# Optimization experiments

Measured on AMD Instinct MI355X. Metric: run time of the kernel, lower is better.

## Reference

```python
import jax, jax.numpy as jnp
import numpy as np

B_, L_, DM, DI, N, R, K = 2, 1024, 1024, 2048, 16, 64, 4
EPS = 1e-5

def silu(x):
    return x * jax.nn.sigmoid(x)

def causal_conv1d(x, w, b):
    # x: (B,L,D); w: (D,K) depthwise. torch Conv1d(padding=K-1) then slice [:L] == left-pad causal conv.
    L = x.shape[1]
    xp = jnp.pad(x, ((0, 0), (K - 1, 0), (0, 0)))
    y = xp[:, 0:L, :] * w[:, 0]
    for k in range(1, K):
        y = y + xp[:, k:k + L, :] * w[:, k]
    return y + b

def selective_scan(u, delta, A, Bm, Cm, D):
    # u, delta: (B,L,D); A: (D,N); Bm, Cm: (B,L,N)
    dA = jnp.exp(jnp.einsum('bld,dn->bldn', delta, A))
    dBu = jnp.einsum('bld,bln,bld->bldn', delta, Bm, u)
    h0 = jnp.zeros((u.shape[0], u.shape[2], A.shape[1]), u.dtype)
    def step(h, xs):
        dA_t, dBu_t, C_t = xs
        h = dA_t * h + dBu_t
        return h, jnp.einsum('bdn,bn->bd', h, C_t)
    _, ys = jax.lax.scan(step, h0, (jnp.moveaxis(dA, 1, 0), jnp.moveaxis(dBu, 1, 0), jnp.moveaxis(Cm, 1, 0)))
    return jnp.moveaxis(ys, 0, 1) + u * D  # (B,L,D)

def branch(x, conv_w, conv_b, Wx, Wdt, bdt, A_log, D):
    x = silu(causal_conv1d(x, conv_w, conv_b))
    dbl = x @ Wx.T                               # (B,L,R+2N)
    dt, Bm, Cm = dbl[..., :R], dbl[..., R:R + N], dbl[..., R + N:]
    dt = dt @ Wdt.T + bdt                        # dt_proj is Linear WITH bias in source
    delta = jax.nn.softplus(dt + bdt)            # source also passes delta_bias to the scan (bias added twice; faithful)
    A = -jnp.exp(A_log)
    return selective_scan(x, delta, A, Bm, Cm, D)

def reference(a, b, Wi, conv_w, conv_b, Wx, Wdt, bdt, A_log, D,
              conv_w_b, conv_b_b, Wx_b, Wdt_b, bdt_b, A_log_b, D_b, Wo, norm_w):
    xz_a = a @ Wi.T
    x_f, z = xz_a[..., :DI], xz_a[..., DI:]
    y_f = branch(x_f, conv_w, conv_b, Wx, Wdt, bdt, A_log, D)
    xz_b = jnp.flip(b, 1) @ Wi.T
    x_bwd = xz_b[..., :DI]
    y_b = jnp.flip(branch(x_bwd, conv_w_b, conv_b_b, Wx_b, Wdt_b, bdt_b, A_log_b, D_b), 1)
    y = y_f + y_b
    # RMSNormGated, norm_before_gate=False: gate first, then RMSNorm
    g = y * silu(z)
    g = g * jax.lax.rsqrt(jnp.mean(g * g, axis=-1, keepdims=True) + EPS) * norm_w
    return g @ Wo.T

def setup_inputs() -> dict:
    key = jax.random.key(0)
    ks = jax.random.split(key, 16)
    s = 0.02
    def rn(k, shape):
        return jax.random.normal(k, shape, jnp.float32) * s
    def inv_dt(k):
        dt = jnp.exp(jax.random.uniform(k, (DI,)) * (np.log(0.1) - np.log(0.001)) + np.log(0.001))
        dt = jnp.clip(dt, 1e-4, None)
        return dt + jnp.log(-jnp.expm1(-dt))
    A_log = jnp.log(jnp.broadcast_to(jnp.arange(1, N + 1, dtype=jnp.float32), (DI, N)))
    return dict(
        a=jax.random.normal(ks[0], (B_, L_, DM), jnp.float32),
        b=jax.random.normal(ks[1], (B_, L_, DM), jnp.float32),
        Wi=rn(ks[2], (2 * DI, DM)),
        conv_w=rn(ks[3], (DI, K)), conv_b=rn(ks[4], (DI,)),
        Wx=rn(ks[5], (R + 2 * N, DI)), Wdt=rn(ks[6], (DI, R)), bdt=inv_dt(ks[7]),
        A_log=A_log, D=jnp.ones((DI,), jnp.float32),
        conv_w_b=rn(ks[8], (DI, K)), conv_b_b=rn(ks[9], (DI,)),
        Wx_b=rn(ks[10], (R + 2 * N, DI)), Wdt_b=rn(ks[11], (DI, R)), bdt_b=inv_dt(ks[12]),
        A_log_b=A_log, D_b=jnp.ones((DI,), jnp.float32),
        Wo=rn(ks[13], (DM, DI)), norm_w=jnp.ones((DI,), jnp.float32),
    )
```

## Files before the change

### kernel.cpp

```cpp
#include <hip/hip_runtime.h>
#include <hip/hip_bf16.h>
#include <cmath>

#define B_ 2
#define L_ 1024
#define DM 1024
#define DI 2048
#define NS 16
#define RR 64
#define KC 4
#define NCH 64
#define CL (L_ / NCH)
#define NSPLIT 16

using frag8 = __attribute__((ext_vector_type(8))) short;
using facc4 = __attribute__((ext_vector_type(4))) float;

struct alignas(8) S4 { short x, y, z, w; };

__device__ __forceinline__ short f2b(float v) {
    __hip_bfloat16 h = __float2bfloat16(v);
    return *(short*)&h;
}

__device__ __forceinline__ float silu1(float x) {
    return x / (1.f + __expf(-x));
}

__device__ __forceinline__ void pow_tree(float q, float* pw) {
    float q2 = q * q, q4 = q2 * q2, q8 = q4 * q4;
    pw[0] = q;        pw[1] = q2;       pw[2] = q2 * q;   pw[3] = q4;
    pw[4] = q4 * q;   pw[5] = q4 * q2;  pw[6] = q4 * pw[2]; pw[7] = q8;
    pw[8] = q8 * q;   pw[9] = q8 * q2;  pw[10] = q8 * pw[2]; pw[11] = q8 * q4;
    pw[12] = q8 * pw[4]; pw[13] = q8 * pw[5]; pw[14] = q8 * pw[6]; pw[15] = q8 * q8;
}

__device__ __forceinline__ void async_ld16(const void* g, void* l) {
    __builtin_amdgcn_global_load_lds(
        (const __attribute__((address_space(1))) unsigned int*)g,
        (__attribute__((address_space(3))) unsigned int*)l, 16, 0, 0);
}

__device__ __forceinline__ void cvt4(const float* __restrict__ src, size_t si,
                                     short* __restrict__ dst, size_t di2) {
    float4 v = *(const float4*)(src + si);
    S4 r = { f2b(v.x), f2b(v.y), f2b(v.z), f2b(v.w) };
    *(S4*)(dst + di2) = r;
}

__global__ void cvt_all(const float* __restrict__ a, const float* __restrict__ b,
                        const float* __restrict__ Wi,
                        const float* __restrict__ Wx, const float* __restrict__ Wxb2,
                        const float* __restrict__ Wdt, const float* __restrict__ Wdtb2,
                        const float* __restrict__ Wo,
                        short* __restrict__ abf, short* __restrict__ bbf,
                        short* __restrict__ Wibf,
                        short* __restrict__ Wxbf, short* __restrict__ Wxbbf,
                        short* __restrict__ Wdtbf, short* __restrict__ Wdtbbf,
                        short* __restrict__ Wobf) {
    size_t i = ((size_t)blockIdx.x * 256 + threadIdx.x) * 4;
    const size_t S_ab = (size_t)B_ * L_ * DM;
    if (i < S_ab) { cvt4(a, i, abf, i); return; } i -= S_ab;
    if (i < S_ab) {
        size_t r = i / DM, c = i % DM;
        size_t bb = r / L_, ll = r % L_;
        size_t sr = bb * L_ + (L_ - 1 - ll);
        cvt4(b, sr * DM + c, bbf, i); return;
    } i -= S_ab;
    const size_t S_wi = (size_t)2 * DI * DM;
    if (i < S_wi) { cvt4(Wi, i, Wibf, i); return; } i -= S_wi;
    const size_t S_wx = (size_t)96 * DI;
    if (i < S_wx) { cvt4(Wx, i, Wxbf, i); return; } i -= S_wx;
    if (i < S_wx) { cvt4(Wxb2, i, Wxbbf, i); return; } i -= S_wx;
    const size_t S_wd = (size_t)DI * RR;
    if (i < S_wd) { cvt4(Wdt, i, Wdtbf, i); return; } i -= S_wd;
    if (i < S_wd) { cvt4(Wdtb2, i, Wdtbbf, i); return; } i -= S_wd;
    const size_t S_wo = (size_t)DM * DI;
    if (i < S_wo) cvt4(Wo, i, Wobf, i);
}

template <int BM>
__device__ __forceinline__ void gemm_body(
    const short* A, int lda, const short* W, int ldw, int wRowOff,
    float* C, int ldc, int K, int m0, int n0) {
    constexpr int MF = BM / 32;
    __shared__ __align__(16) short As[2][BM * 32];
    __shared__ __align__(16) short Ws[2][64 * 32];
    const int tid = threadIdx.x;
    const int lane = tid & 63, wv = tid >> 6;
    const int wm = (wv & 1) * (BM / 2), wn = (wv >> 1) * 32;
    const int q = lane >> 4, mr = lane & 15;
    const int srow = lane >> 2, skb = lane & 3;

    const short* Ag = A + (size_t)(m0 + wv * 16 + srow) * lda + skb * 8;
    const short* Wg = W + (size_t)(n0 + wRowOff + wv * 16 + srow) * ldw + skb * 8;

    facc4 acc[MF][2];
#pragma unroll
    for (int i = 0; i < MF; ++i)
#pragma unroll
        for (int j = 0; j < 2; ++j) acc[i][j] = (facc4){0.f, 0.f, 0.f, 0.f};

    async_ld16(Ag, &As[0][wv * 512]);
    if constexpr (BM == 128) async_ld16(Ag + (size_t)64 * lda, &As[0][wv * 512 + 2048]);
    async_ld16(Wg, &Ws[0][wv * 512]);

    const int nk = K / 32;
    for (int it = 0; it < nk; ++it) {
        const int buf = it & 1;
        __syncthreads();
        if (it + 1 < nk) {
            int k0 = (it + 1) * 32;
            async_ld16(Ag + k0, &As[buf ^ 1][wv * 512]);
            if constexpr (BM == 128)
                async_ld16(Ag + (size_t)64 * lda + k0, &As[buf ^ 1][wv * 512 + 2048]);
            async_ld16(Wg + k0, &Ws[buf ^ 1][wv * 512]);
        }
        frag8 af[MF], wf[2];
#pragma unroll
        for (int t = 0; t < MF; ++t)
            af[t] = *(const frag8*)&As[buf][((wm + t * 16 + mr) * 4 + q) * 8];
#pragma unroll
        for (int j = 0; j < 2; ++j)
            wf[j] = *(const frag8*)&Ws[buf][((wn + j * 16 + mr) * 4 + q) * 8];
#pragma unroll
        for (int i = 0; i < MF; ++i)
#pragma unroll
            for (int j = 0; j < 2; ++j)
                acc[i][j] = __builtin_amdgcn_mfma_f32_16x16x32_bf16(af[i], wf[j], acc[i][j], 0, 0, 0);
    }
#pragma unroll
    for (int i = 0; i < MF; ++i)
#pragma unroll
        for (int j = 0; j < 2; ++j) {
            int gn = n0 + wn + j * 16 + mr;
#pragma unroll
            for (int e = 0; e < 4; ++e) {
                int gm = m0 + wm + i * 16 + q * 4 + e;
                C[(size_t)gm * ldc + gn] = acc[i][j][e];
            }
        }
}

__global__ __launch_bounds__(256) void gemm_xz(
    const short* __restrict__ abf, const short* __restrict__ bbf,
    const short* __restrict__ Wibf,
    float* __restrict__ XF, float* __restrict__ XB, float* __restrict__ Z) {
    const int bz = blockIdx.z;
    const short* A = (bz == 1) ? bbf : abf;
    float* C = (bz == 0) ? XF : (bz == 1) ? XB : Z;
    const int off = (bz == 2) ? DI : 0;
    gemm_body<128>(A, DM, Wibf, DM, off, C, DI, DM, blockIdx.y * 128, blockIdx.x * 64);
}

__global__ __launch_bounds__(256) void gemm_dt(
    const short* __restrict__ dtf, const short* __restrict__ dtb,
    const short* __restrict__ Wf, const short* __restrict__ Wb,
    float* __restrict__ DTF_, float* __restrict__ DTB_) {
    const int bz = blockIdx.z;
    gemm_body<64>(bz ? dtb : dtf, RR, bz ? Wb : Wf, RR, 0,
                  bz ? DTB_ : DTF_, DI, RR, blockIdx.y * 64, blockIdx.x * 64);
}

__global__ __launch_bounds__(256) void gemm_out(
    const short* __restrict__ gbf, const short* __restrict__ Wobf,
    float* __restrict__ out) {
    gemm_body<64>(gbf, DI, Wobf, DI, 0, out, DM, DI, blockIdx.y * 64, blockIdx.x * 64);
}

__global__ __launch_bounds__(256) void gemm_dbl(
    const short* __restrict__ CF, const short* __restrict__ CB,
    const short* __restrict__ Wxf, const short* __restrict__ Wxb,
    float* __restrict__ part) {
    __shared__ __align__(16) short As[2][128 * 32];
    __shared__ __align__(16) short Ws[2][96 * 32];
    const int br = blockIdx.z / NSPLIT, zz = blockIdx.z % NSPLIT;
    const short* A = br ? CB : CF;
    const short* W = br ? Wxb : Wxf;
    constexpr int Kchunk = DI / NSPLIT;
    const int tid = threadIdx.x;
    const int lane = tid & 63, wv = tid >> 6;
    const int m0 = blockIdx.y * 128;
    const int kOff = zz * Kchunk;
    const int wm = (wv & 1) * 64, wn = (wv >> 1) * 48;
    const int q = lane >> 4, mr = lane & 15;
    const int srow = lane >> 2, skb = lane & 3;

    const short* Ag = A + (size_t)(m0 + wv * 16 + srow) * DI + skb * 8 + kOff;
    const short* Wg = W + (size_t)(wv * 16 + srow) * DI + skb * 8 + kOff;

    facc4 acc[4][3];
#pragma unroll
    for (int i = 0; i < 4; ++i)
#pragma unroll
        for (int j = 0; j < 3; ++j) acc[i][j] = (facc4){0.f, 0.f, 0.f, 0.f};

    async_ld16(Ag, &As[0][wv * 512]);
    async_ld16(Ag + (size_t)64 * DI, &As[0][wv * 512 + 2048]);
    async_ld16(Wg, &Ws[0][wv * 512]);
    if (wv < 2) async_ld16(Wg + (size_t)64 * DI, &Ws[0][wv * 512 + 2048]);

    const int nk = Kchunk / 32;
    for (int it = 0; it < nk; ++it) {
        const int buf = it & 1;
        __syncthreads();
        if (it + 1 < nk) {
            int k0 = (it + 1) * 32;
            async_ld16(Ag + k0, &As[buf ^ 1][wv * 512]);
            async_ld16(Ag + (size_t)64 * DI + k0, &As[buf ^ 1][wv * 512 + 2048]);
            async_ld16(Wg + k0, &Ws[buf ^ 1][wv * 512]);
            if (wv < 2) async_ld16(Wg + (size_t)64 * DI + k0, &Ws[buf ^ 1][wv * 512 + 2048]);
        }
        frag8 af[4], wf[3];
#pragma unroll
        for (int t = 0; t < 4; ++t)
            af[t] = *(const frag8*)&As[buf][((wm + t * 16 + mr) * 4 + q) * 8];
#pragma unroll
        for (int j = 0; j < 3; ++j)
            wf[j] = *(const frag8*)&Ws[buf][((wn + j * 16 + mr) * 4 + q) * 8];
#pragma unroll
        for (int i = 0; i < 4; ++i)
#pragma unroll
            for (int j = 0; j < 3; ++j)
                acc[i][j] = __builtin_amdgcn_mfma_f32_16x16x32_bf16(af[i], wf[j], acc[i][j], 0, 0, 0);
    }
    float* Cz = part + (size_t)blockIdx.z * (B_ * L_) * 96;
#pragma unroll
    for (int i = 0; i < 4; ++i)
#pragma unroll
        for (int j = 0; j < 3; ++j) {
            int gn = wn + j * 16 + mr;
#pragma unroll
            for (int e = 0; e < 4; ++e) {
                int gm = m0 + wm + i * 16 + q * 4 + e;
                Cz[(size_t)gm * 96 + gn] = acc[i][j][e];
            }
        }
}

__global__ void reduce_dbl(const float* __restrict__ part,
                           float* __restrict__ dblf, float* __restrict__ dblb,
                           short* __restrict__ dtf, short* __restrict__ dtb) {
    int idx = blockIdx.x * blockDim.x + threadIdx.x;
    const int T = B_ * L_ * 96;
    int br = 0;
    if (idx >= T) { br = 1; idx -= T; }
    const float* p = part + (size_t)br * NSPLIT * T;
    float s = 0.f;
#pragma unroll
    for (int z = 0; z < NSPLIT; ++z) s += p[(size_t)z * T + idx];
    (br ? dblb : dblf)[idx] = s;
    int row = idx / 96, col = idx % 96;
    if (col < RR) (br ? dtb : dtf)[(size_t)row * RR + col] = f2b(s);
}

__global__ void conv_silu2(const float* __restrict__ XF, const float* __restrict__ XB,
                           const float* __restrict__ cwf, const float* __restrict__ cbff,
                           const float* __restrict__ cwb, const float* __restrict__ cbbb,
                           float* __restrict__ UF, float* __restrict__ UB,
                           short* __restrict__ CFo, short* __restrict__ CBo) {
    size_t idx = ((size_t)blockIdx.x * 256 + threadIdx.x) * 4;
    const size_t T = (size_t)B_ * L_ * DI;
    int br = 0;
    if (idx >= T) { br = 1; idx -= T; }
    const float* __restrict__ x = br ? XB : XF;
    const float* __restrict__ w = br ? cwb : cwf;
    const float* __restrict__ bias = br ? cbbb : cbff;
    float* __restrict__ y = br ? UB : UF;
    short* __restrict__ ybf = br ? CBo : CFo;
    int d = (int)(idx % DI);
    int l = (int)((idx / DI) % L_);
    float wl[16];
    *(float4*)&wl[0]  = *(const float4*)(w + (size_t)d * KC);
    *(float4*)&wl[4]  = *(const float4*)(w + (size_t)(d + 1) * KC);
    *(float4*)&wl[8]  = *(const float4*)(w + (size_t)(d + 2) * KC);
    *(float4*)&wl[12] = *(const float4*)(w + (size_t)(d + 3) * KC);
    float4 acc = *(const float4*)(bias + d);
#pragma unroll
    for (int k = 0; k < KC; ++k) {
        int ls = l + k - (KC - 1);
        if (ls >= 0) {
            float4 xv = *(const float4*)(x + idx + (size_t)(ls - l) * DI);
            acc.x = fmaf(xv.x, wl[0 + k], acc.x);
            acc.y = fmaf(xv.y, wl[4 + k], acc.y);
            acc.z = fmaf(xv.z, wl[8 + k], acc.z);
            acc.w = fmaf(xv.w, wl[12 + k], acc.w);
        }
    }
    float4 v = { silu1(acc.x), silu1(acc.y), silu1(acc.z), silu1(acc.w) };
    *(float4*)(y + idx) = v;
    S4 o = { f2b(v.x), f2b(v.y), f2b(v.z), f2b(v.w) };
    *(S4*)(ybf + idx) = o;
}

__device__ __forceinline__ float softplus2(float raw, float bd2) {
    float x = raw + bd2;
    return (x > 20.f) ? x : log1pf(__expf(x));
}

__global__ void scan_chunk(float* UF, float* UB, float* DTFm, float* DTBm,
                           const float* bdtf, const float* bdtb,
                           const float* dblF, const float* dblB,
                           const float* Alf, const float* Alb,
                           const float* Dvf, const float* Dvb,
                           float* PF, float* SF, float* PB, float* SB) {
    __shared__ float BCs[CL][32];
    const int tid = threadIdx.x;
    const int d = blockIdx.x * 256 + tid;
    const int br = blockIdx.y >> 1, bb = blockIdx.y & 1;
    const int c = blockIdx.z;
    const int l0 = c * CL;
    float* __restrict__ u = br ? UB : UF;
    float* __restrict__ dtm = br ? DTBm : DTFm;
    const float* __restrict__ bdt = br ? bdtb : bdtf;
    const float* __restrict__ dbl = br ? dblB : dblF;
    const float* __restrict__ A_log = br ? Alb : Alf;
    const float* __restrict__ Dv = br ? Dvb : Dvf;
    float* __restrict__ Pbuf = br ? PB : PF;
    float* __restrict__ Sbuf = br ? SB : SF;
    {
        int e = tid * 2;
        int row = e >> 5, cc = e & 31;
        *(float2*)&BCs[row][cc] =
            *(const float2*)(dbl + ((size_t)(bb * L_ + l0 + row) * 96 + 64 + cc));
    }
    float Av[NS], S[NS];
#pragma unroll
    for (int n = 0; n < NS; ++n) { Av[n] = -__expf(A_log[d * NS + n]); S[n] = 0.f; }
    bool structured = true;
#pragma unroll
    for (int n = 1; n < NS; ++n)
        structured = structured &&
            (fabsf(Av[n] - (n + 1) * Av[0]) <= 1e-4f * (n + 1) * fabsf(Av[0]));
    const float bd2 = 2.f * bdt[d];
    const float Dd = Dv[d];
    float cd = 0.f;
    __syncthreads();
    float* __restrict__ up = u + ((size_t)bb * L_ + l0) * DI + d;
    float* __restrict__ dp = dtm + ((size_t)bb * L_ + l0) * DI + d;
    float draw = dp[0], ul = up[0];
    if (structured) {
        const float Av0 = Av[0];
        for (int l = 0; l < CL; ++l) {
            float draw_n = 0.f, ul_n = 0.f;
            if (l + 1 < CL) { draw_n = dp[(size_t)(l + 1) * DI]; ul_n = up[(size_t)(l + 1) * DI]; }
            float del = softplus2(draw, bd2);
            cd += del;
            float du = del * ul;
            float pw[NS];
            pow_tree(__expf(del * Av0), pw);
            const float* Brow = &BCs[l][0];
            float pa[4] = {0.f, 0.f, 0.f, 0.f};
#pragma unroll
            for (int j = 0; j < 4; ++j)
#pragma unroll
                for (int k = 0; k < 4; ++k) {
                    int n = j * 4 + k;
                    S[n] = fmaf(pw[n], S[n], du * Brow[n]);
                    pa[j] = fmaf(S[n], Brow[16 + n], pa[j]);
                }
            float acc = (pa[0] + pa[1]) + (pa[2] + pa[3]);
            dp[(size_t)l * DI] = cd;
            up[(size_t)l * DI] = acc + ul * Dd;
            draw = draw_n; ul = ul_n;
        }
    } else {
        for (int l = 0; l < CL; ++l) {
            float draw_n = 0.f, ul_n = 0.f;
            if (l + 1 < CL) { draw_n = dp[(size_t)(l + 1) * DI]; ul_n = up[(size_t)(l + 1) * DI]; }
            float del = softplus2(draw, bd2);
            cd += del;
            float du = del * ul;
            const float* Brow = &BCs[l][0];
            float pa[4] = {0.f, 0.f, 0.f, 0.f};
#pragma unroll
            for (int j = 0; j < 4; ++j)
#pragma unroll
                for (int k = 0; k < 4; ++k) {
                    int n = j * 4 + k;
                    float dA = __expf(del * Av[n]);
                    S[n] = fmaf(dA, S[n], du * Brow[n]);
                    pa[j] = fmaf(S[n], Brow[16 + n], pa[j]);
                }
            float acc = (pa[0] + pa[1]) + (pa[2] + pa[3]);
            dp[(size_t)l * DI] = cd;
            up[(size_t)l * DI] = acc + ul * Dd;
            draw = draw_n; ul = ul_n;
        }
    }
    size_t pb = ((size_t)(bb * NCH + c) * NS) * DI + d;
    if (structured) {
        float pw[NS];
        pow_tree(__expf(cd * Av[0]), pw);
#pragma unroll
        for (int n = 0; n < NS; ++n) {
            Pbuf[pb + (size_t)n * DI] = pw[n];
            Sbuf[pb + (size_t)n * DI] = S[n];
        }
    } else {
#pragma unroll
        for (int n = 0; n < NS; ++n) {
            Pbuf[pb + (size_t)n * DI] = __expf(cd * Av[n]);
            Sbuf[pb + (size_t)n * DI] = S[n];
        }
    }
}

__global__ void scan_combine(float* __restrict__ PF, const float* __restrict__ SF,
                             float* __restrict__ PB, const float* __restrict__ SB) {
    int g = blockIdx.x * blockDim.x + threadIdx.x;
    const int T = B_ * NS * DI;
    float* __restrict__ P = (g < T) ? PF : PB;
    const float* __restrict__ S = (g < T) ? SF : SB;
    int gg = (g < T) ? g : g - T;
    int d = gg % DI;
    int rest = gg / DI;
    int n = rest % NS, bb = rest / NS;
    const size_t stride = (size_t)NS * DI;
    size_t o = ((size_t)(bb * NCH) * NS + n) * DI + d;
    float h = 0.f;
    float Pc = P[o], Sc = S[o];
    for (int c = 0; c < NCH; ++c) {
        float Pn = 0.f, Sn = 0.f;
        if (c + 1 < NCH) { Pn = P[o + stride]; Sn = S[o + stride]; }
        P[o] = h;
        h = fmaf(Pc, h, Sc);
        Pc = Pn; Sc = Sn;
        o += stride;
    }
}

__global__ void scan_apply(float* UF, float* UB,
                           const float* DTFm, const float* DTBm,
                           const float* dblF, const float* dblB,
                           const float* Alf, const float* Alb,
                           const float* PF, const float* PB) {
    __shared__ float Cs[CL][16];
    const int tid = threadIdx.x;
    const int d = blockIdx.x * 256 + tid;
    const int br = blockIdx.y >> 1, bb = blockIdx.y & 1;
    const int c = blockIdx.z + 1;
    const int l0 = c * CL;
    float* __restrict__ y = br ? UB : UF;
    const float* __restrict__ cdm = br ? DTBm : DTFm;
    const float* __restrict__ dbl = br ? dblB : dblF;
    const float* __restrict__ A_log = br ? Alb : Alf;
    const float* __restrict__ Hbuf = br ? PB : PF;
    {
        int row = tid >> 4, cc = tid & 15;
        Cs[row][cc] = dbl[(size_t)(bb * L_ + l0 + row) * 96 + 80 + cc];
    }
    float Av[NS], chs[NS];
#pragma unroll
    for (int n = 0; n < NS; ++n) Av[n] = -__expf(A_log[d * NS + n]);
    bool structured = true;
#pragma unroll
    for (int n = 1; n < NS; ++n)
        structured = structured &&
            (fabsf(Av[n] - (n + 1) * Av[0]) <= 1e-4f * (n + 1) * fabsf(Av[0]));
    size_t pb = ((size_t)(bb * NCH + c) * NS) * DI + d;
#pragma unroll
    for (int n = 0; n < NS; ++n) chs[n] = Hbuf[pb + (size_t)n * DI];
    __syncthreads();
    const float* __restrict__ cp = cdm + ((size_t)bb * L_ + l0) * DI + d;
    float* __restrict__ yp = y + ((size_t)bb * L_ + l0) * DI + d;
    float cdv = cp[0], yv = yp[0];
    if (structured) {
        const float Av0 = Av[0];
        for (int l = 0; l < CL; ++l) {
            float cdn = 0.f, yn = 0.f;
            if (l + 1 < CL) { cdn = cp[(size_t)(l + 1) * DI]; yn = yp[(size_t)(l + 1) * DI]; }
            float pw[NS];
            pow_tree(__expf(cdv * Av0), pw);
            const float* Crow = &Cs[l][0];
            float pa[4] = {0.f, 0.f, 0.f, 0.f};
#pragma unroll
            for (int j = 0; j < 4; ++j)
#pragma unroll
                for (int k = 0; k < 4; ++k) {
                    int n = j * 4 + k;
                    pa[j] = fmaf(pw[n], Crow[n] * chs[n], pa[j]);
                }
            yp[(size_t)l * DI] = yv + (pa[0] + pa[1]) + (pa[2] + pa[3]);
            cdv = cdn; yv = yn;
        }
    } else {
        for (int l = 0; l < CL; ++l) {
            float cdn = 0.f, yn = 0.f;
            if (l + 1 < CL) { cdn = cp[(size_t)(l + 1) * DI]; yn = yp[(size_t)(l + 1) * DI]; }
            const float* Crow = &Cs[l][0];
            float pa[4] = {0.f, 0.f, 0.f, 0.f};
#pragma unroll
            for (int j = 0; j < 4; ++j)
#pragma unroll
                for (int k = 0; k < 4; ++k) {
                    int n = j * 4 + k;
                    pa[j] = fmaf(__expf(cdv * Av[n]), Crow[n] * chs[n], pa[j]);
                }
            yp[(size_t)l * DI] = yv + (pa[0] + pa[1]) + (pa[2] + pa[3]);
            cdv = cdn; yv = yn;
        }
    }
}

__global__ void combine_rms(const float* __restrict__ yf, const float* __restrict__ yb,
                            const float* __restrict__ z,
                            const float* __restrict__ nw,
                            short* __restrict__ g) {
    int row = blockIdx.x;
    int bb = row / L_, l = row % L_;
    int tid = threadIdx.x;
    size_t base = (size_t)row * DI;
    size_t baseb = ((size_t)bb * L_ + (L_ - 1 - l)) * DI;
    float4 gv[2];
    float ss = 0.f;
#pragma unroll
    for (int j = 0; j < 2; ++j) {
        int d = tid * 4 + j * 1024;
        float4 a4 = *(const float4*)(yf + base + d);
        float4 b4 = *(const float4*)(yb + baseb + d);
        float4 z4 = *(const float4*)(z + base + d);
        float4 r;
        r.x = (a4.x + b4.x) * silu1(z4.x);
        r.y = (a4.y + b4.y) * silu1(z4.y);
        r.z = (a4.z + b4.z) * silu1(z4.z);
        r.w = (a4.w + b4.w) * silu1(z4.w);
        gv[j] = r;
        ss += r.x * r.x + r.y * r.y + r.z * r.z + r.w * r.w;
    }
#pragma unroll
    for (int off = 32; off > 0; off >>= 1) ss += __shfl_down(ss, off, 64);
    __shared__ float red[4];
    if ((tid & 63) == 0) red[tid >> 6] = ss;
    __syncthreads();
    float tot = red[0] + red[1] + red[2] + red[3];
    float rms = rsqrtf(tot / (float)DI + 1e-5f);
#pragma unroll
    for (int j = 0; j < 2; ++j) {
        int d = tid * 4 + j * 1024;
        float4 w4 = *(const float4*)(nw + d);
        S4 o = { f2b(gv[j].x * rms * w4.x), f2b(gv[j].y * rms * w4.y),
                 f2b(gv[j].z * rms * w4.z), f2b(gv[j].w * rms * w4.w) };
        *(S4*)(g + base + d) = o;
    }
}

extern "C" void kernel_launch(void* const* d_in, const int* in_sizes, int n_in,
                              void* d_out, int out_size, void* d_ws, size_t ws_size,
                              hipStream_t stream) {
    const float* a      = (const float*)d_in[0];
    const float* b      = (const float*)d_in[1];
    const float* Wi     = (const float*)d_in[2];
    const float* conv_w = (const float*)d_in[3];
    const float* conv_b = (const float*)d_in[4];
    const float* Wx     = (const float*)d_in[5];
    const float* Wdt    = (const float*)d_in[6];
    const float* bdt    = (const float*)d_in[7];
    const float* A_log  = (const float*)d_in[8];
    const float* Dvec   = (const float*)d_in[9];
    const float* conv_w_b = (const float*)d_in[10];
    const float* conv_b_b = (const float*)d_in[11];
    const float* Wx_b   = (const float*)d_in[12];
    const float* Wdt_b  = (const float*)d_in[13];
    const float* bdt_b  = (const float*)d_in[14];
    const float* A_log_b = (const float*)d_in[15];
    const float* Dvec_b = (const float*)d_in[16];
    const float* Wo     = (const float*)d_in[17];
    const float* nw     = (const float*)d_in[18];
    float* out = (float*)d_out;

    const int M = B_ * L_;
    const size_t BLD = (size_t)M * DI;
    const size_t NDBL = (size_t)M * 96;
    const size_t PSsz = (size_t)NCH * B_ * NS * DI;

    float* f = (float*)d_ws;
    float* XF   = f;  f += BLD;
    float* XB   = f;  f += BLD;
    float* Zb   = f;  f += BLD;
    float* UF   = f;  f += BLD;
    float* UB   = f;  f += BLD;
    float* DTF  = f;  f += BLD;
    float* DTB  = f;  f += BLD;
    float* dblf = f;  f += NDBL;
    float* dblb = f;  f += NDBL;
    float* Pf   = f;  f += PSsz;
    float* Sf   = f;  f += PSsz;
    float* Pb   = f;  f += PSsz;
    float* Sb   = f;  f += PSsz;
    float* part = Pf;

    short* s = (short*)f;
    short* abf    = s;  s += (size_t)M * DM;
    short* bbf    = s;  s += (size_t)M * DM;
    short* Wibf   = s;  s += (size_t)2 * DI * DM;
    short* CF     = s;  s += BLD;
    short* CB     = s;  s += BLD;
    short* Wxbf   = s;  s += (size_t)96 * DI;
    short* Wxbbf  = s;  s += (size_t)96 * DI;
    short* Wdtbf  = s;  s += (size_t)DI * RR;
    short* Wdtbbf = s;  s += (size_t)DI * RR;
    short* dtfbf  = s;  s += (size_t)M * RR;
    short* dtbbf  = s;  s += (size_t)M * RR;
    short* Wobf   = s;  s += (size_t)DM * DI;
    short* gbf    = abf;

    dim3 blk(256);

    cvt_all<<<dim3(10880), blk, 0, stream>>>(a, b, Wi, Wx, Wx_b, Wdt, Wdt_b, Wo,
                                             abf, bbf, Wibf, Wxbf, Wxbbf, Wdtbf, Wdtbbf, Wobf);
    gemm_xz<<<dim3(DI / 64, M / 128, 3), blk, 0, stream>>>(abf, bbf, Wibf, XF, XB, Zb);
    conv_silu2<<<dim3(2 * (int)(BLD / 1024)), blk, 0, stream>>>(
        XF, XB, conv_w, conv_b, conv_w_b, conv_b_b, UF, UB, CF, CB);
    gemm_dbl<<<dim3(1, M / 128, 2 * NSPLIT), blk, 0, stream>>>(CF, CB, Wxbf, Wxbbf, part);
    reduce_dbl<<<dim3(2 * (int)(NDBL / 256)), blk, 0, stream>>>(part, dblf, dblb, dtfbf, dtbbf);
    gemm_dt<<<dim3(DI / 64, M / 64, 2), blk, 0, stream>>>(dtfbf, dtbbf, Wdtbf, Wdtbbf, DTF, DTB);
    scan_chunk<<<dim3(DI / 256, 4, NCH), blk, 0, stream>>>(
        UF, UB, DTF, DTB, bdt, bdt_b, dblf, dblb, A_log, A_log_b, Dvec, Dvec_b,
        Pf, Sf, Pb, Sb);
    scan_combine<<<dim3(2 * B_ * NS * DI / 256), blk, 0, stream>>>(Pf, Sf, Pb, Sb);
    scan_apply<<<dim3(DI / 256, 4, NCH - 1), blk, 0, stream>>>(
        UF, UB, DTF, DTB, dblf, dblb, A_log, A_log_b, Pf, Pb);
    combine_rms<<<dim3(M), blk, 0, stream>>>(UF, UB, Zb, nw, gbf);
    gemm_out<<<dim3(DM / 64, M / 64), blk, 0, stream>>>(gbf, Wobf, out);
}
```

Before: 343.2 us.

## Fuse causal conv+SiLU into input GEMM epilogue and vectorize scan state

The in-projection GEMM now performs the depthwise causal conv and SiLU in its epilogue. It recomputes a 16-row halo with extra MFMAs so each block can handle the left context at chunk boundaries, which removes the XF/XB fp32 round trip and the separate conv kernel. The chunked scan kernels now hold state in float4 vector types with vectorized shared-memory reads, and scan_combine prefetches four chunks at a time. The cost is extra halo MFMA work, more shared memory in the GEMM, and a more complex epilogue that could reduce occupancy.

```diff
diff --git a/kernel.cpp b/kernel.cpp
--- a/kernel.cpp
+++ b/kernel.cpp
@@ -15,8 +15,9 @@
 
 using frag8 = __attribute__((ext_vector_type(8))) short;
 using facc4 = __attribute__((ext_vector_type(4))) float;
-
-struct alignas(8) S4 { short x, y, z, w; };
+using f32x4 = __attribute__((ext_vector_type(4))) float;
+
+struct alignas(8) S4v { short x, y, z, w; };
 
 __device__ __forceinline__ short f2b(float v) {
     __hip_bfloat16 h = __float2bfloat16(v);
@@ -27,12 +28,14 @@
     return x / (1.f + __expf(-x));
 }
 
-__device__ __forceinline__ void pow_tree(float q, float* pw) {
-    float q2 = q * q, q4 = q2 * q2, q8 = q4 * q4;
-    pw[0] = q;        pw[1] = q2;       pw[2] = q2 * q;   pw[3] = q4;
-    pw[4] = q4 * q;   pw[5] = q4 * q2;  pw[6] = q4 * pw[2]; pw[7] = q8;
-    pw[8] = q8 * q;   pw[9] = q8 * q2;  pw[10] = q8 * pw[2]; pw[11] = q8 * q4;
-    pw[12] = q8 * pw[4]; pw[13] = q8 * pw[5]; pw[14] = q8 * pw[6]; pw[15] = q8 * q8;
+__device__ __forceinline__ void pow4(float qv, f32x4& p0, f32x4& p1, f32x4& p2, f32x4& p3) {
+    float q2 = qv * qv, q3 = q2 * qv, q4 = q2 * q2;
+    p0 = (f32x4){qv, q2, q3, q4};
+    f32x4 s4 = {q4, q4, q4, q4};
+    p1 = p0 * s4;
+    f32x4 s8 = s4 * s4;
+    p2 = p0 * s8;
+    p3 = p1 * s8;
 }
 
 __device__ __forceinline__ void async_ld16(const void* g, void* l) {
@@ -44,8 +47,8 @@
 __device__ __forceinline__ void cvt4(const float* __restrict__ src, size_t si,
                                      short* __restrict__ dst, size_t di2) {
     float4 v = *(const float4*)(src + si);
-    S4 r = { f2b(v.x), f2b(v.y), f2b(v.z), f2b(v.w) };
-    *(S4*)(dst + di2) = r;
+    S4v r = { f2b(v.x), f2b(v.y), f2b(v.z), f2b(v.w) };
+    *(S4v*)(dst + di2) = r;
 }
 
 __global__ void cvt_all(const float* __restrict__ a, const float* __restrict__ b,
@@ -142,15 +145,154 @@
         }
 }
 
-__global__ __launch_bounds__(256) void gemm_xz(
+__global__ __launch_bounds__(256) void gemm_xz_conv(
     const short* __restrict__ abf, const short* __restrict__ bbf,
     const short* __restrict__ Wibf,
-    float* __restrict__ XF, float* __restrict__ XB, float* __restrict__ Z) {
+    float* __restrict__ UF, float* __restrict__ UB, float* __restrict__ Z,
+    short* __restrict__ CFo, short* __restrict__ CBo,
+    const float* __restrict__ cwf, const float* __restrict__ cbf2,
+    const float* __restrict__ cwb, const float* __restrict__ cbb2) {
+    __shared__ __align__(16) char smem[26624];
+    short (*As)[144 * 32] = (short (*)[144 * 32])smem;
+    short (*Ws)[64 * 32]  = (short (*)[64 * 32])(smem + 18432);
+    float (*Xs)[65] = (float (*)[65])smem;
+
     const int bz = blockIdx.z;
+    const bool isX = (bz != 2);
+    const int tid = threadIdx.x;
+    const int lane = tid & 63, wv = tid >> 6;
+    const int m0 = blockIdx.y * 128, n0 = blockIdx.x * 64;
+    const bool hasHalo = isX && (m0 % L_ != 0);
+    const int wm = (wv & 1) * 64, wn = (wv >> 1) * 32;
+    const int q = lane >> 4, mr = lane & 15;
+    const int srow = lane >> 2, skb = lane & 3;
+
     const short* A = (bz == 1) ? bbf : abf;
-    float* C = (bz == 0) ? XF : (bz == 1) ? XB : Z;
-    const int off = (bz == 2) ? DI : 0;
-    gemm_body<128>(A, DM, Wibf, DM, off, C, DI, DM, blockIdx.y * 128, blockIdx.x * 64);
+    const int wOff = (bz == 2) ? DI : 0;
+
+    const short* Ag  = A + (size_t)(m0 + wv * 16 + srow) * DM + skb * 8;
+    const short* Agh = A + (size_t)(m0 - 16 + srow) * DM + skb * 8;
+    const short* Wg  = Wibf + (size_t)(n0 + wOff + wv * 16 + srow) * DM + skb * 8;
+
+    facc4 acc[4][2], hacc[2];
+#pragma unroll
+    for (int i = 0; i < 4; ++i)
+#pragma unroll
+        for (int j = 0; j < 2; ++j) acc[i][j] = (facc4){0.f, 0.f, 0.f, 0.f};
+#pragma unroll
+    for (int j = 0; j < 2; ++j) hacc[j] = (facc4){0.f, 0.f, 0.f, 0.f};
+
+    async_ld16(Ag, &As[0][wv * 512]);
+    async_ld16(Ag + (size_t)64 * DM, &As[0][wv * 512 + 2048]);
+    async_ld16(Wg, &Ws[0][wv * 512]);
+    if (hasHalo && wv == 0) async_ld16(Agh, &As[0][4096]);
+
+    const int nk = DM / 32;
+    for (int it = 0; it < nk; ++it) {
+        const int buf = it & 1;
+        __syncthreads();
+        if (it + 1 < nk) {
+            int k0 = (it + 1) * 32;
+            async_ld16(Ag + k0, &As[buf ^ 1][wv * 512]);
+            async_ld16(Ag + (size_t)64 * DM + k0, &As[buf ^ 1][wv * 512 + 2048]);
+            async_ld16(Wg + k0, &Ws[buf ^ 1][wv * 512]);
+            if (hasHalo && wv == 0) async_ld16(Agh + k0, &As[buf ^ 1][4096]);
+        }
+        frag8 af[4], wf[2];
+#pragma unroll
+        for (int t = 0; t < 4; ++t)
+            af[t] = *(const frag8*)&As[buf][((wm + t * 16 + mr) * 4 + q) * 8];
+#pragma unroll
+        for (int j = 0; j < 2; ++j)
+            wf[j] = *(const frag8*)&Ws[buf][((wn + j * 16 + mr) * 4 + q) * 8];
+        if (hasHalo && wm == 0) {
+            frag8 afh = *(const frag8*)&As[buf][((128 + mr) * 4 + q) * 8];
+#pragma unroll
+            for (int j = 0; j < 2; ++j)
+                hacc[j] = __builtin_amdgcn_mfma_f32_16x16x32_bf16(afh, wf[j], hacc[j], 0, 0, 0);
+        }
+#pragma unroll
+        for (int i = 0; i < 4; ++i)
+#pragma unroll
+            for (int j = 0; j < 2; ++j)
+                acc[i][j] = __builtin_amdgcn_mfma_f32_16x16x32_bf16(af[i], wf[j], acc[i][j], 0, 0, 0);
+    }
+
+    if (!isX) {
+#pragma unroll
+        for (int i = 0; i < 4; ++i)
+#pragma unroll
+            for (int j = 0; j < 2; ++j) {
+                int gn = n0 + wn + j * 16 + mr;
+#pragma unroll
+                for (int e = 0; e < 4; ++e) {
+                    int gm = m0 + wm + i * 16 + q * 4 + e;
+                    Z[(size_t)gm * DI + gn] = acc[i][j][e];
+                }
+            }
+        return;
+    }
+
+    const float* cw = (bz == 1) ? cwb : cwf;
+    const float* cb = (bz == 1) ? cbb2 : cbf2;
+    float* U   = (bz == 1) ? UB : UF;
+    short* Co  = (bz == 1) ? CBo : CFo;
+    const int col = tid & 63;
+    const int dcol = n0 + col;
+    const int rg = tid >> 6;
+    float4 wd = *(const float4*)(cw + (size_t)dcol * KC);
+    float bd = cb[dcol];
+
+    __syncthreads();
+#pragma unroll
+    for (int p = 0; p < 2; ++p) {
+        if (p == 0) {
+            if ((wv & 1) == 0) {
+#pragma unroll
+                for (int j = 0; j < 2; ++j) {
+#pragma unroll
+                    for (int e = 0; e < 4; ++e)
+                        Xs[q * 4 + e][wn + j * 16 + mr] = hacc[j][e];
+#pragma unroll
+                    for (int i = 0; i < 4; ++i)
+#pragma unroll
+                        for (int e = 0; e < 4; ++e)
+                            Xs[16 + i * 16 + q * 4 + e][wn + j * 16 + mr] = acc[i][j][e];
+                }
+            }
+        } else {
+            if ((wv & 1) == 0) {
+#pragma unroll
+                for (int j = 0; j < 2; ++j)
+#pragma unroll
+                    for (int e = 0; e < 4; ++e)
+                        Xs[q * 4 + e][wn + j * 16 + mr] = acc[3][j][e];
+            } else {
+#pragma unroll
+                for (int j = 0; j < 2; ++j)
+#pragma unroll
+                    for (int i = 0; i < 4; ++i)
+#pragma unroll
+                        for (int e = 0; e < 4; ++e)
+                            Xs[16 + i * 16 + q * 4 + e][wn + j * 16 + mr] = acc[i][j][e];
+            }
+        }
+        __syncthreads();
+#pragma unroll
+        for (int rr = 0; rr < 16; ++rr) {
+            int rl = rg * 16 + rr;
+            float x0 = Xs[13 + rl][col];
+            float x1 = Xs[14 + rl][col];
+            float x2 = Xs[15 + rl][col];
+            float x3 = Xs[16 + rl][col];
+            float v = bd + x0 * wd.x + x1 * wd.y + x2 * wd.z + x3 * wd.w;
+            float s2 = silu1(v);
+            size_t go = (size_t)(m0 + p * 64 + rl) * DI + dcol;
+            U[go] = s2;
+            Co[go] = f2b(s2);
+        }
+        if (p == 0) __syncthreads();
+    }
 }
 
 __global__ __launch_bounds__(256) void gemm_dt(
@@ -254,45 +396,6 @@
     if (col < RR) (br ? dtb : dtf)[(size_t)row * RR + col] = f2b(s);
 }
 
-__global__ void conv_silu2(const float* __restrict__ XF, const float* __restrict__ XB,
-                           const float* __restrict__ cwf, const float* __restrict__ cbff,
-                           const float* __restrict__ cwb, const float* __restrict__ cbbb,
-                           float* __restrict__ UF, float* __restrict__ UB,
-                           short* __restrict__ CFo, short* __restrict__ CBo) {
-    size_t idx = ((size_t)blockIdx.x * 256 + threadIdx.x) * 4;
-    const size_t T = (size_t)B_ * L_ * DI;
-    int br = 0;
-    if (idx >= T) { br = 1; idx -= T; }
-    const float* __restrict__ x = br ? XB : XF;
-    const float* __restrict__ w = br ? cwb : cwf;
-    const float* __restrict__ bias = br ? cbbb : cbff;
-    float* __restrict__ y = br ? UB : UF;
-    short* __restrict__ ybf = br ? CBo : CFo;
-    int d = (int)(idx % DI);
-    int l = (int)((idx / DI) % L_);
-    float wl[16];
-    *(float4*)&wl[0]  = *(const float4*)(w + (size_t)d * KC);
-    *(float4*)&wl[4]  = *(const float4*)(w + (size_t)(d + 1) * KC);
-    *(float4*)&wl[8]  = *(const float4*)(w + (size_t)(d + 2) * KC);
-    *(float4*)&wl[12] = *(const float4*)(w + (size_t)(d + 3) * KC);
-    float4 acc = *(const float4*)(bias + d);
-#pragma unroll
-    for (int k = 0; k < KC; ++k) {
-        int ls = l + k - (KC - 1);
-        if (ls >= 0) {
-            float4 xv = *(const float4*)(x + idx + (size_t)(ls - l) * DI);
-            acc.x = fmaf(xv.x, wl[0 + k], acc.x);
-            acc.y = fmaf(xv.y, wl[4 + k], acc.y);
-            acc.z = fmaf(xv.z, wl[8 + k], acc.z);
-            acc.w = fmaf(xv.w, wl[12 + k], acc.w);
-        }
-    }
-    float4 v = { silu1(acc.x), silu1(acc.y), silu1(acc.z), silu1(acc.w) };
-    *(float4*)(y + idx) = v;
-    S4 o = { f2b(v.x), f2b(v.y), f2b(v.z), f2b(v.w) };
-    *(S4*)(ybf + idx) = o;
-}
-
 __device__ __forceinline__ float softplus2(float raw, float bd2) {
     float x = raw + bd2;
     return (x > 20.f) ? x : log1pf(__expf(x));
@@ -304,7 +407,7 @@
                            const float* Alf, const float* Alb,
                            const float* Dvf, const float* Dvb,
                            float* PF, float* SF, float* PB, float* SB) {
-    __shared__ float BCs[CL][32];
+    __shared__ __align__(16) float BCs[CL][32];
     const int tid = threadIdx.x;
     const int d = blockIdx.x * 256 + tid;
     const int br = blockIdx.y >> 1, bb = blockIdx.y & 1;
@@ -324,9 +427,9 @@
         *(float2*)&BCs[row][cc] =
             *(const float2*)(dbl + ((size_t)(bb * L_ + l0 + row) * 96 + 64 + cc));
     }
-    float Av[NS], S[NS];
-#pragma unroll
-    for (int n = 0; n < NS; ++n) { Av[n] = -__expf(A_log[d * NS + n]); S[n] = 0.f; }
+    float Av[NS];
+#pragma unroll
+    for (int n = 0; n < NS; ++n) Av[n] = -__expf(A_log[d * NS + n]);
     bool structured = true;
 #pragma unroll
     for (int n = 1; n < NS; ++n)
@@ -338,33 +441,55 @@
     __syncthreads();
     float* __restrict__ up = u + ((size_t)bb * L_ + l0) * DI + d;
     float* __restrict__ dp = dtm + ((size_t)bb * L_ + l0) * DI + d;
-    float draw = dp[0], ul = up[0];
+    size_t pb = ((size_t)(bb * NCH + c) * NS) * DI + d;
+
     if (structured) {
         const float Av0 = Av[0];
+        f32x4 S4[4];
+#pragma unroll
+        for (int m = 0; m < 4; ++m) S4[m] = (f32x4){0.f, 0.f, 0.f, 0.f};
+        float draw = dp[0], ul = up[0];
         for (int l = 0; l < CL; ++l) {
             float draw_n = 0.f, ul_n = 0.f;
             if (l + 1 < CL) { draw_n = dp[(size_t)(l + 1) * DI]; ul_n = up[(size_t)(l + 1) * DI]; }
-            float del = softplus2(draw, bd2);
+            float x = draw + bd2;
+            float e = __expf(x);
+            float del = (x > 20.f) ? x : __logf(1.f + e);
             cd += del;
             float du = del * ul;
-            float pw[NS];
-            pow_tree(__expf(del * Av0), pw);
-            const float* Brow = &BCs[l][0];
-            float pa[4] = {0.f, 0.f, 0.f, 0.f};
-#pragma unroll
-            for (int j = 0; j < 4; ++j)
-#pragma unroll
-                for (int k = 0; k < 4; ++k) {
-                    int n = j * 4 + k;
-                    S[n] = fmaf(pw[n], S[n], du * Brow[n]);
-                    pa[j] = fmaf(S[n], Brow[16 + n], pa[j]);
-                }
-            float acc = (pa[0] + pa[1]) + (pa[2] + pa[3]);
+            f32x4 pw0, pw1, pw2, pw3;
+            pow4(__expf(del * Av0), pw0, pw1, pw2, pw3);
+            const f32x4* BC4 = (const f32x4*)&BCs[l][0];
+            f32x4 b0 = BC4[0], b1 = BC4[1], b2 = BC4[2], b3 = BC4[3];
+            f32x4 c0 = BC4[4], c1 = BC4[5], c2 = BC4[6], c3 = BC4[7];
+            f32x4 du4 = {du, du, du, du};
+            S4[0] = pw0 * S4[0] + du4 * b0;
+            S4[1] = pw1 * S4[1] + du4 * b1;
+            S4[2] = pw2 * S4[2] + du4 * b2;
+            S4[3] = pw3 * S4[3] + du4 * b3;
+            f32x4 pA = S4[0] * c0 + S4[1] * c1;
+            f32x4 pB = S4[2] * c2 + S4[3] * c3;
+            f32x4 pv = pA + pB;
+            float accv = (pv[0] + pv[1]) + (pv[2] + pv[3]);
             dp[(size_t)l * DI] = cd;
-            up[(size_t)l * DI] = acc + ul * Dd;
+            up[(size_t)l * DI] = accv + ul * Dd;
             draw = draw_n; ul = ul_n;
         }
+        f32x4 pw0, pw1, pw2, pw3;
+        pow4(__expf(cd * Av0), pw0, pw1, pw2, pw3);
+        f32x4 pws[4] = {pw0, pw1, pw2, pw3};
+#pragma unroll
+        for (int m = 0; m < 4; ++m)
+#pragma unroll
+            for (int k2 = 0; k2 < 4; ++k2) {
+                Pbuf[pb + (size_t)(m * 4 + k2) * DI] = pws[m][k2];
+                Sbuf[pb + (size_t)(m * 4 + k2) * DI] = S4[m][k2];
+            }
     } else {
+        float S[NS];
+#pragma unroll
+        for (int n = 0; n < NS; ++n) S[n] = 0.f;
+        float draw = dp[0], ul = up[0];
         for (int l = 0; l < CL; ++l) {
             float draw_n = 0.f, ul_n = 0.f;
             if (l + 1 < CL) { draw_n = dp[(size_t)(l + 1) * DI]; ul_n = up[(size_t)(l + 1) * DI]; }
@@ -382,22 +507,11 @@
                     S[n] = fmaf(dA, S[n], du * Brow[n]);
                     pa[j] = fmaf(S[n], Brow[16 + n], pa[j]);
                 }
-            float acc = (pa[0] + pa[1]) + (pa[2] + pa[3]);
+            float accv = (pa[0] + pa[1]) + (pa[2] + pa[3]);
             dp[(size_t)l * DI] = cd;
-            up[(size_t)l * DI] = acc + ul * Dd;
+            up[(size_t)l * DI] = accv + ul * Dd;
             draw = draw_n; ul = ul_n;
         }
-    }
-    size_t pb = ((size_t)(bb * NCH + c) * NS) * DI + d;
-    if (structured) {
-        float pw[NS];
-        pow_tree(__expf(cd * Av[0]), pw);
-#pragma unroll
-        for (int n = 0; n < NS; ++n) {
-            Pbuf[pb + (size_t)n * DI] = pw[n];
-            Sbuf[pb + (size_t)n * DI] = S[n];
-        }
-    } else {
 #pragma unroll
         for (int n = 0; n < NS; ++n) {
             Pbuf[pb + (size_t)n * DI] = __expf(cd * Av[n]);
@@ -419,14 +533,25 @@
     const size_t stride = (size_t)NS * DI;
     size_t o = ((size_t)(bb * NCH) * NS + n) * DI + d;
     float h = 0.f;
-    float Pc = P[o], Sc = S[o];
-    for (int c = 0; c < NCH; ++c) {
-        float Pn = 0.f, Sn = 0.f;
-        if (c + 1 < NCH) { Pn = P[o + stride]; Sn = S[o + stride]; }
-        P[o] = h;
-        h = fmaf(Pc, h, Sc);
-        Pc = Pn; Sc = Sn;
-        o += stride;
+    float Pc[4], Sc[4], Pn[4], Sn[4];
+#pragma unroll
+    for (int i = 0; i < 4; ++i) { Pc[i] = P[o + (size_t)i * stride]; Sc[i] = S[o + (size_t)i * stride]; }
+    for (int c = 0; c < NCH; c += 4) {
+        if (c + 4 < NCH) {
+#pragma unroll
+            for (int i = 0; i < 4; ++i) {
+                Pn[i] = P[o + (size_t)(i + 4) * stride];
+                Sn[i] = S[o + (size_t)(i + 4) * stride];
+            }
+        }
+#pragma unroll
+        for (int i = 0; i < 4; ++i) {
+            P[o] = h;
+            h = fmaf(Pc[i], h, Sc[i]);
+            o += stride;
+        }
+#pragma unroll
+        for (int i = 0; i < 4; ++i) { Pc[i] = Pn[i]; Sc[i] = Sn[i]; }
     }
 }
 
@@ -435,7 +560,7 @@
                            const float* dblF, const float* dblB,
                            const float* Alf, const float* Alb,
                            const float* PF, const float* PB) {
-    __shared__ float Cs[CL][16];
+    __shared__ __align__(16) float Cs[CL][16];
     const int tid = threadIdx.x;
     const int d = blockIdx.x * 256 + tid;
     const int br = blockIdx.y >> 1, bb = blockIdx.y & 1;
@@ -450,7 +575,7 @@
         int row = tid >> 4, cc = tid & 15;
         Cs[row][cc] = dbl[(size_t)(bb * L_ + l0 + row) * 96 + 80 + cc];
     }
-    float Av[NS], chs[NS];
+    float Av[NS];
 #pragma unroll
     for (int n = 0; n < NS; ++n) Av[n] = -__expf(A_log[d * NS + n]);
     bool structured = true;
@@ -459,32 +584,37 @@
         structured = structured &&
             (fabsf(Av[n] - (n + 1) * Av[0]) <= 1e-4f * (n + 1) * fabsf(Av[0]));
     size_t pb = ((size_t)(bb * NCH + c) * NS) * DI + d;
-#pragma unroll
-    for (int n = 0; n < NS; ++n) chs[n] = Hbuf[pb + (size_t)n * DI];
-    __syncthreads();
     const float* __restrict__ cp = cdm + ((size_t)bb * L_ + l0) * DI + d;
     float* __restrict__ yp = y + ((size_t)bb * L_ + l0) * DI + d;
-    float cdv = cp[0], yv = yp[0];
+
     if (structured) {
+        f32x4 ch4[4];
+#pragma unroll
+        for (int m = 0; m < 4; ++m)
+#pragma unroll
+            for (int k2 = 0; k2 < 4; ++k2)
+                ch4[m][k2] = Hbuf[pb + (size_t)(m * 4 + k2) * DI];
+        __syncthreads();
         const float Av0 = Av[0];
+        float cdv = cp[0], yv = yp[0];
         for (int l = 0; l < CL; ++l) {
             float cdn = 0.f, yn = 0.f;
             if (l + 1 < CL) { cdn = cp[(size_t)(l + 1) * DI]; yn = yp[(size_t)(l + 1) * DI]; }
-            float pw[NS];
-            pow_tree(__expf(cdv * Av0), pw);
-            const float* Crow = &Cs[l][0];
-            float pa[4] = {0.f, 0.f, 0.f, 0.f};
-#pragma unroll
-            for (int j = 0; j < 4; ++j)
-#pragma unroll
-                for (int k = 0; k < 4; ++k) {
-                    int n = j * 4 + k;
-                    pa[j] = fmaf(pw[n], Crow[n] * chs[n], pa[j]);
-                }
-            yp[(size_t)l * DI] = yv + (pa[0] + pa[1]) + (pa[2] + pa[3]);
+            f32x4 pw0, pw1, pw2, pw3;
+            pow4(__expf(cdv * Av0), pw0, pw1, pw2, pw3);
+            const f32x4* C4 = (const f32x4*)&Cs[l][0];
+            f32x4 pA = pw0 * (C4[0] * ch4[0]) + pw1 * (C4[1] * ch4[1]);
+            f32x4 pB = pw2 * (C4[2] * ch4[2]) + pw3 * (C4[3] * ch4[3]);
+            f32x4 pv = pA + pB;
+            yp[(size_t)l * DI] = yv + (pv[0] + pv[1]) + (pv[2] + pv[3]);
             cdv = cdn; yv = yn;
         }
     } else {
+        float chs[NS];
+#pragma unroll
+        for (int n = 0; n < NS; ++n) chs[n] = Hbuf[pb + (size_t)n * DI];
+        __syncthreads();
+        float cdv = cp[0], yv = yp[0];
         for (int l = 0; l < CL; ++l) {
             float cdn = 0.f, yn = 0.f;
             if (l + 1 < CL) { cdn = cp[(size_t)(l + 1) * DI]; yn = yp[(size_t)(l + 1) * DI]; }
@@ -539,9 +669,9 @@
     for (int j = 0; j < 2; ++j) {
         int d = tid * 4 + j * 1024;
         float4 w4 = *(const float4*)(nw + d);
-        S4 o = { f2b(gv[j].x * rms * w4.x), f2b(gv[j].y * rms * w4.y),
-                 f2b(gv[j].z * rms * w4.z), f2b(gv[j].w * rms * w4.w) };
-        *(S4*)(g + base + d) = o;
+        S4v o = { f2b(gv[j].x * rms * w4.x), f2b(gv[j].y * rms * w4.y),
+                  f2b(gv[j].z * rms * w4.z), f2b(gv[j].w * rms * w4.w) };
+        *(S4v*)(g + base + d) = o;
     }
 }
 
@@ -575,8 +705,6 @@
     const size_t PSsz = (size_t)NCH * B_ * NS * DI;
 
     float* f = (float*)d_ws;
-    float* XF   = f;  f += BLD;
-    float* XB   = f;  f += BLD;
     float* Zb   = f;  f += BLD;
     float* UF   = f;  f += BLD;
     float* UB   = f;  f += BLD;
@@ -609,9 +737,9 @@
 
     cvt_all<<<dim3(10880), blk, 0, stream>>>(a, b, Wi, Wx, Wx_b, Wdt, Wdt_b, Wo,
                                              abf, bbf, Wibf, Wxbf, Wxbbf, Wdtbf, Wdtbbf, Wobf);
-    gemm_xz<<<dim3(DI / 64, M / 128, 3), blk, 0, stream>>>(abf, bbf, Wibf, XF, XB, Zb);
-    conv_silu2<<<dim3(2 * (int)(BLD / 1024)), blk, 0, stream>>>(
-        XF, XB, conv_w, conv_b, conv_w_b, conv_b_b, UF, UB, CF, CB);
+    gemm_xz_conv<<<dim3(DI / 64, M / 128, 3), blk, 0, stream>>>(
+        abf, bbf, Wibf, UF, UB, Zb, CF, CB,
+        conv_w, conv_b, conv_w_b, conv_b_b);
     gemm_dbl<<<dim3(1, M / 128, 2 * NSPLIT), blk, 0, stream>>>(CF, CB, Wxbf, Wxbbf, part);
     reduce_dbl<<<dim3(2 * (int)(NDBL / 256)), blk, 0, stream>>>(part, dblf, dblb, dtfbf, dtbbf);
     gemm_dt<<<dim3(DI / 64, M / 64, 2), blk, 0, stream>>>(dtfbf, dtbbf, Wdtbf, Wdtbbf, DTF, DTB);
```

Measured after the change: 298.6 us. 13.0% less time.
